# Optimization experiments

Hardware: AMD Instinct MI355X
Metric: run time of the kernel (lower is better)

## Reference

```python
import jax, jax.numpy as jnp
import numpy as np

NUM_HEADS = 4
HEAD_DIM = 64  # out_dim // num_heads = 256 // 4
NEG_SLOPE = 0.2


def setup_inputs() -> dict:
    key = jax.random.key(0)
    k1, k2 = jax.random.split(key)
    h = jax.random.normal(k1, (8, 2048, 256), dtype=jnp.float32)
    # Linear(in_dim, head_dim*num_heads, bias=False): store as [in_dim, out_dim]
    W = jax.random.normal(k2, (256, 256), dtype=jnp.float32) * (1.0 / np.sqrt(256.0))
    return {"h": h, "W": W}


def reference(h, W):
    B, T, _ = h.shape
    # Wh: (B, H, T, D)
    Wh = (h @ W).reshape(B, T, NUM_HEADS, HEAD_DIM).transpose(0, 2, 1, 3)
    scale = 1.0 / (HEAD_DIM ** 0.5)
    # full T x T scores per head, LeakyReLU then softmax over keys
    scores = jnp.einsum('bhtd,bhsd->bhts', Wh, Wh) * scale
    attention = jax.nn.softmax(jax.nn.leaky_relu(scores, negative_slope=NEG_SLOPE), axis=-1)
    h_prime = jnp.einsum('bhts,bhsd->bhtd', attention, Wh)
    # concat=True: (B, T, H*D)
    return h_prime.transpose(0, 2, 1, 3).reshape(B, T, NUM_HEADS * HEAD_DIM)
```

## Files before the change

kernel.cpp:

```cpp
#include <hip/hip_runtime.h>

#define T_SEQ 2048
#define NH 4
#define DH 64

typedef __bf16 bf16x8 __attribute__((ext_vector_type(8)));
typedef float f32x4 __attribute__((ext_vector_type(4)));
typedef unsigned short u16x8 __attribute__((ext_vector_type(8)));

__device__ __forceinline__ unsigned short f2bf_rne(float x) {
  unsigned int u = __builtin_bit_cast(unsigned int, x);
  u += 0x7fffu + ((u >> 16) & 1u);
  return (unsigned short)(u >> 16);
}
__device__ __forceinline__ float bf2f(unsigned short s) {
  unsigned int u = ((unsigned int)s) << 16;
  return __builtin_bit_cast(float, u);
}

__global__ void prep_w(const float* __restrict__ W,
                       unsigned short* __restrict__ WtHi,
                       unsigned short* __restrict__ WtLo) {
  __shared__ float ls[32][65];
  const int tid = threadIdx.x;
  const int k0 = (blockIdx.x >> 2) * 32;
  const int n0 = (blockIdx.x & 3) * 64;
#pragma unroll
  for (int i = 0; i < 8; i++) {
    int e = i * 256 + tid;
    int r = e >> 6, c = e & 63;
    ls[r][c] = W[(k0 + r) * 256 + n0 + c];
  }
  __syncthreads();
  const int n = tid & 63;
  const int part = tid >> 6;
  u16x8 vh, vl;
#pragma unroll
  for (int j = 0; j < 8; j++) {
    float w = ls[part * 8 + j][n];
    unsigned short h16 = f2bf_rne(w);
    vh[j] = h16;
    vl[j] = f2bf_rne(w - bf2f(h16));
  }
  size_t dst = (size_t)(n0 + n) * 256 + k0 + part * 8;
  *(u16x8*)&WtHi[dst] = vh;
  *(u16x8*)&WtLo[dst] = vl;
}

__global__ __launch_bounds__(256, 2) void wh_gemm(
    const float* __restrict__ h,
    const unsigned short* __restrict__ WtHi,
    const unsigned short* __restrict__ WtLo,
    unsigned short* __restrict__ Kb, unsigned short* __restrict__ Vs) {
  __shared__ __align__(16) unsigned short ktile[32][272];
  __shared__ __align__(16) unsigned short vtile[256][40];
  const int tid = threadIdx.x;
  const int wave = tid >> 6, lane = tid & 63, l15 = lane & 15, quad = lane >> 4;
  const int m0b = blockIdx.x * 32;
  const int m0 = m0b + (wave & 1) * 16;
  const int n0w = (wave >> 1) * 128;
  f32x4 acc[8];
#pragma unroll
  for (int nt = 0; nt < 8; nt++) acc[nt] = (f32x4){0.f, 0.f, 0.f, 0.f};

  for (int kc = 0; kc < 8; kc++) {
    const float4* hp = (const float4*)&h[(size_t)(m0 + l15) * 256 + kc * 32 + quad * 8];
    float4 a0 = hp[0], a1 = hp[1];
    float xs[8] = {a0.x, a0.y, a0.z, a0.w, a1.x, a1.y, a1.z, a1.w};
    u16x8 ah, al;
#pragma unroll
    for (int j = 0; j < 8; j++) {
      unsigned short h16 = f2bf_rne(xs[j]);
      ah[j] = h16;
      al[j] = f2bf_rne(xs[j] - bf2f(h16));
    }
    bf16x8 ahi = __builtin_bit_cast(bf16x8, ah);
    bf16x8 alo = __builtin_bit_cast(bf16x8, al);
#pragma unroll
    for (int nt = 0; nt < 8; nt++) {
      size_t wb = (size_t)(n0w + nt * 16 + l15) * 256 + kc * 32 + quad * 8;
      bf16x8 bhi = *(const bf16x8*)&WtHi[wb];
      bf16x8 blo = *(const bf16x8*)&WtLo[wb];
      acc[nt] = __builtin_amdgcn_mfma_f32_16x16x32_bf16(ahi, bhi, acc[nt], 0, 0, 0);
      acc[nt] = __builtin_amdgcn_mfma_f32_16x16x32_bf16(alo, bhi, acc[nt], 0, 0, 0);
      acc[nt] = __builtin_amdgcn_mfma_f32_16x16x32_bf16(ahi, blo, acc[nt], 0, 0, 0);
    }
  }
  const float s1 = 0.424664717f;
  const int tl = (wave & 1) * 16 + quad * 4;
#pragma unroll
  for (int nt = 0; nt < 8; nt++) {
    int n = n0w + nt * 16 + l15;
    ushort4 vp;
#pragma unroll
    for (int r = 0; r < 4; r++) {
      float v = acc[nt][r];
      ktile[tl + r][n] = f2bf_rne(v * s1);
      ((unsigned short*)&vp)[r] = f2bf_rne(v);
    }
    *(uint2*)&vtile[n][tl] = __builtin_bit_cast(uint2, vp);
  }
  __syncthreads();
  {
    int t = tid >> 3, seg = tid & 7;
    int m = m0b + t, b = m >> 11, tt = m & 2047;
    int head = seg >> 1, d0 = (seg & 1) * 32;
    unsigned short* dst = &Kb[((size_t)(b * NH + head) * T_SEQ + tt) * DH + d0];
#pragma unroll
    for (int q = 0; q < 4; q++)
      *(u16x8*)&dst[q * 8] = *(const u16x8*)&ktile[t][seg * 32 + q * 8];
  }
  {
    int n = tid, head = n >> 6, d = n & 63;
    int b = m0b >> 11, t0 = m0b & 2047;
    unsigned short* dst = &Vs[((size_t)(b * NH + head) * DH + d) * T_SEQ + t0];
#pragma unroll
    for (int q = 0; q < 4; q++) {
      uint2 lo = *(const uint2*)&vtile[n][q * 4];
      uint2 hi = *(const uint2*)&vtile[n][16 + q * 4];
      uint4 pk = {lo.x, lo.y, hi.x, hi.y};
      *(uint4*)&dst[q * 8] = pk;
    }
  }
}

__global__ __launch_bounds__(256, 3) void attn(
    const unsigned short* __restrict__ Kb, const unsigned short* __restrict__ Vs,
    float* __restrict__ out) {
  __shared__ __align__(16) float cbuf[2][64 * 68];
  __shared__ float lbuf[4][64];
  __shared__ float inv_s[64];
  const int tid = threadIdx.x, wave = tid >> 6, lane = tid & 63;
  const int l15 = lane & 15, quad = lane >> 4;
  const int bh = blockIdx.x & 31;
  const int qt = blockIdx.x >> 5;
  const int q0 = qt * 64;
  const unsigned short* Kbh = Kb + (size_t)bh * T_SEQ * DH;
  const unsigned short* Vbh = Vs + (size_t)bh * DH * T_SEQ;

  bf16x8 bq[4][2];
#pragma unroll
  for (int nt = 0; nt < 4; nt++)
#pragma unroll
    for (int kc = 0; kc < 2; kc++)
      bq[nt][kc] = *(const bf16x8*)&Kbh[(size_t)(q0 + nt * 16 + l15) * DH + kc * 32 + quad * 8];

  f32x4 o[4][4];
  float lsum[4] = {0.f, 0.f, 0.f, 0.f};
#pragma unroll
  for (int mt = 0; mt < 4; mt++)
#pragma unroll
    for (int dt = 0; dt < 4; dt++) o[mt][dt] = (f32x4){0.f, 0.f, 0.f, 0.f};

  const int sbase = wave * 512;
  bf16x8 ka[2][2], vb[4];
#pragma unroll
  for (int mt = 0; mt < 2; mt++)
#pragma unroll
    for (int kc = 0; kc < 2; kc++)
      ka[mt][kc] = *(const bf16x8*)&Kbh[(size_t)(sbase + mt * 16 + l15) * DH + kc * 32 + quad * 8];
#pragma unroll
  for (int dt = 0; dt < 4; dt++)
    vb[dt] = *(const bf16x8*)&Vbh[(size_t)(dt * 16 + l15) * T_SEQ + sbase + quad * 8];

  for (int it = 0; it < 16; it++) {
    const int nxt = sbase + ((it == 15) ? it : it + 1) * 32;
    f32x4 s[2][4];
#pragma unroll
    for (int mt = 0; mt < 2; mt++)
#pragma unroll
      for (int nt = 0; nt < 4; nt++) {
        f32x4 c = {0.f, 0.f, 0.f, 0.f};
        c = __builtin_amdgcn_mfma_f32_16x16x32_bf16(ka[mt][0], bq[nt][0], c, 0, 0, 0);
        c = __builtin_amdgcn_mfma_f32_16x16x32_bf16(ka[mt][1], bq[nt][1], c, 0, 0, 0);
        s[mt][nt] = c;
      }
#pragma unroll
    for (int mt = 0; mt < 2; mt++)
#pragma unroll
      for (int kc = 0; kc < 2; kc++)
        ka[mt][kc] = *(const bf16x8*)&Kbh[(size_t)(nxt + mt * 16 + l15) * DH + kc * 32 + quad * 8];

    uint2 pk[2][4];
#pragma unroll
    for (int mt = 0; mt < 2; mt++)
#pragma unroll
      for (int nt = 0; nt < 4; nt++) {
        float v0 = s[mt][nt][0], v1 = s[mt][nt][1];
        float v2 = s[mt][nt][2], v3 = s[mt][nt][3];
        float e0 = __builtin_amdgcn_exp2f(fmaxf(v0, 0.2f * v0));
        float e1 = __builtin_amdgcn_exp2f(fmaxf(v1, 0.2f * v1));
        float e2 = __builtin_amdgcn_exp2f(fmaxf(v2, 0.2f * v2));
        float e3 = __builtin_amdgcn_exp2f(fmaxf(v3, 0.2f * v3));
        lsum[nt] += (e0 + e1) + (e2 + e3);
        pk[mt][nt].x = (__builtin_bit_cast(unsigned int, e1) & 0xffff0000u) |
                       (__builtin_bit_cast(unsigned int, e0) >> 16);
        pk[mt][nt].y = (__builtin_bit_cast(unsigned int, e3) & 0xffff0000u) |
                       (__builtin_bit_cast(unsigned int, e2) >> 16);
      }

#pragma unroll
    for (int mq = 0; mq < 4; mq++) {
      uint4 pu = {pk[0][mq].x, pk[0][mq].y, pk[1][mq].x, pk[1][mq].y};
      bf16x8 pa = __builtin_bit_cast(bf16x8, pu);
#pragma unroll
      for (int dt = 0; dt < 4; dt++)
        o[mq][dt] = __builtin_amdgcn_mfma_f32_16x16x32_bf16(pa, vb[dt], o[mq][dt], 0, 0, 0);
    }
#pragma unroll
    for (int dt = 0; dt < 4; dt++)
      vb[dt] = *(const bf16x8*)&Vbh[(size_t)(dt * 16 + l15) * T_SEQ + nxt + quad * 8];
  }

#pragma unroll
  for (int nt = 0; nt < 4; nt++) {
    float l = lsum[nt];
    l += __shfl_xor(l, 16, 64);
    l += __shfl_xor(l, 32, 64);
    if (quad == 0) lbuf[wave][nt * 16 + l15] = l;
  }
  __syncthreads();
  if (wave >= 2) {
    float* cb = cbuf[wave - 2];
#pragma unroll
    for (int mt = 0; mt < 4; mt++)
#pragma unroll
      for (int dt = 0; dt < 4; dt++)
        *(f32x4*)&cb[(dt * 16 + l15) * 68 + mt * 16 + quad * 4] = o[mt][dt];
  }
  if (wave == 0) {
    float s = lbuf[0][lane] + lbuf[1][lane] + lbuf[2][lane] + lbuf[3][lane];
    inv_s[lane] = 1.0f / s;
  }
  __syncthreads();
  if (wave < 2) {
    float* cb = cbuf[wave];
#pragma unroll
    for (int mt = 0; mt < 4; mt++)
#pragma unroll
      for (int dt = 0; dt < 4; dt++)
        o[mt][dt] += *(const f32x4*)&cb[(dt * 16 + l15) * 68 + mt * 16 + quad * 4];
  }
  __syncthreads();
  if (wave == 1) {
#pragma unroll
    for (int mt = 0; mt < 4; mt++)
#pragma unroll
      for (int dt = 0; dt < 4; dt++)
        *(f32x4*)&cbuf[0][(dt * 16 + l15) * 68 + mt * 16 + quad * 4] = o[mt][dt];
  }
  __syncthreads();
  if (wave == 0) {
#pragma unroll
    for (int mt = 0; mt < 4; mt++)
#pragma unroll
      for (int dt = 0; dt < 4; dt++)
        o[mt][dt] += *(const f32x4*)&cbuf[0][(dt * 16 + l15) * 68 + mt * 16 + quad * 4];
    const int b = bh >> 2, head = bh & 3;
#pragma unroll
    for (int mt = 0; mt < 4; mt++) {
#pragma unroll
      for (int r = 0; r < 4; r++) {
        int q = mt * 16 + quad * 4 + r;
        float iv = inv_s[q];
        float* dst = &out[((size_t)b * T_SEQ + q0 + q) * 256 + head * 64];
#pragma unroll
        for (int dt = 0; dt < 4; dt++) dst[dt * 16 + l15] = o[mt][dt][r] * iv;
      }
    }
  }
}

extern "C" void kernel_launch(void* const* d_in, const int* in_sizes, int n_in,
                              void* d_out, int out_size, void* d_ws, size_t ws_size,
                              hipStream_t stream) {
  const float* h = (const float*)d_in[0];
  const float* W = (const float*)d_in[1];
  float* out = (float*)d_out;
  unsigned short* Kb = (unsigned short*)d_ws;
  unsigned short* Vs = Kb + (size_t)32 * T_SEQ * DH;
  unsigned short* WtHi = (unsigned short*)out;
  unsigned short* WtLo = WtHi + 65536;
  prep_w<<<32, 256, 0, stream>>>(W, WtHi, WtLo);
  wh_gemm<<<512, 256, 0, stream>>>(h, WtHi, WtLo, Kb, Vs);
  attn<<<1024, 256, 0, stream>>>(Kb, Vs, out);
}
```

Measured before the change: 182.0 us.

## Switch attention to fp16 MFMA with fixed exp shift and MFMA row sums

K and V are now stored as fp16 instead of bf16, and the attention kernel uses f16 MFMA. A constant shift of -14 is seeded into the score accumulator (scaled by 0.2 on the negative branch) so the exponentials stay within fp16 range, and they are packed with cvt_pkrtz instead of manual bit truncation. The per-lane scalar row-sum adds and shuffle reduction are replaced by an extra MFMA against a ones vector, whose result goes through the same cross-wave LDS reduction as the output. This trims VALU work in the softmax inner loop and adds one MFMA per query tile, but it relies on the fixed shift keeping fp16 from overflowing or underflowing for these input ranges.

```diff
diff --git a/kernel.cpp b/kernel.cpp
--- a/kernel.cpp
+++ b/kernel.cpp
@@ -5,6 +5,8 @@
 #define DH 64
 
 typedef __bf16 bf16x8 __attribute__((ext_vector_type(8)));
+typedef _Float16 f16x8 __attribute__((ext_vector_type(8)));
+typedef _Float16 f16x2 __attribute__((ext_vector_type(2)));
 typedef float f32x4 __attribute__((ext_vector_type(4)));
 typedef unsigned short u16x8 __attribute__((ext_vector_type(8)));
 
@@ -16,6 +18,10 @@
 __device__ __forceinline__ float bf2f(unsigned short s) {
   unsigned int u = ((unsigned int)s) << 16;
   return __builtin_bit_cast(float, u);
+}
+__device__ __forceinline__ unsigned short f2h(float x) {
+  _Float16 h = (_Float16)x;
+  return __builtin_bit_cast(unsigned short, h);
 }
 
 __global__ void prep_w(const float* __restrict__ W,
@@ -95,8 +101,8 @@
 #pragma unroll
     for (int r = 0; r < 4; r++) {
       float v = acc[nt][r];
-      ktile[tl + r][n] = f2bf_rne(v * s1);
-      ((unsigned short*)&vp)[r] = f2bf_rne(v);
+      ktile[tl + r][n] = f2h(v * s1);
+      ((unsigned short*)&vp)[r] = f2h(v);
     }
     *(uint2*)&vtile[n][tl] = __builtin_bit_cast(uint2, vp);
   }
@@ -127,9 +133,7 @@
 __global__ __launch_bounds__(256, 3) void attn(
     const unsigned short* __restrict__ Kb, const unsigned short* __restrict__ Vs,
     float* __restrict__ out) {
-  __shared__ __align__(16) float cbuf[2][64 * 68];
-  __shared__ float lbuf[4][64];
-  __shared__ float inv_s[64];
+  __shared__ __align__(16) float cbuf[2][80 * 68];
   const int tid = threadIdx.x, wave = tid >> 6, lane = tid & 63;
   const int l15 = lane & 15, quad = lane >> 4;
   const int bh = blockIdx.x & 31;
@@ -138,30 +142,36 @@
   const unsigned short* Kbh = Kb + (size_t)bh * T_SEQ * DH;
   const unsigned short* Vbh = Vs + (size_t)bh * DH * T_SEQ;
 
-  bf16x8 bq[4][2];
+  f16x8 bq[4][2];
 #pragma unroll
   for (int nt = 0; nt < 4; nt++)
 #pragma unroll
     for (int kc = 0; kc < 2; kc++)
-      bq[nt][kc] = *(const bf16x8*)&Kbh[(size_t)(q0 + nt * 16 + l15) * DH + kc * 32 + quad * 8];
-
-  f32x4 o[4][4];
-  float lsum[4] = {0.f, 0.f, 0.f, 0.f};
-#pragma unroll
-  for (int mt = 0; mt < 4; mt++)
+      bq[nt][kc] = *(const f16x8*)&Kbh[(size_t)(q0 + nt * 16 + l15) * DH + kc * 32 + quad * 8];
+
+  f16x8 ones;
+#pragma unroll
+  for (int j = 0; j < 8; j++) ones[j] = (_Float16)1.0f;
+
+  f32x4 o[4][4], lacc[4];
+#pragma unroll
+  for (int mt = 0; mt < 4; mt++) {
+    lacc[mt] = (f32x4){0.f, 0.f, 0.f, 0.f};
 #pragma unroll
     for (int dt = 0; dt < 4; dt++) o[mt][dt] = (f32x4){0.f, 0.f, 0.f, 0.f};
+  }
+  const f32x4 cinit = {-14.f, -14.f, -14.f, -14.f};
 
   const int sbase = wave * 512;
-  bf16x8 ka[2][2], vb[4];
+  f16x8 ka[2][2], vb[4];
 #pragma unroll
   for (int mt = 0; mt < 2; mt++)
 #pragma unroll
     for (int kc = 0; kc < 2; kc++)
-      ka[mt][kc] = *(const bf16x8*)&Kbh[(size_t)(sbase + mt * 16 + l15) * DH + kc * 32 + quad * 8];
+      ka[mt][kc] = *(const f16x8*)&Kbh[(size_t)(sbase + mt * 16 + l15) * DH + kc * 32 + quad * 8];
 #pragma unroll
   for (int dt = 0; dt < 4; dt++)
-    vb[dt] = *(const bf16x8*)&Vbh[(size_t)(dt * 16 + l15) * T_SEQ + sbase + quad * 8];
+    vb[dt] = *(const f16x8*)&Vbh[(size_t)(dt * 16 + l15) * T_SEQ + sbase + quad * 8];
 
   for (int it = 0; it < 16; it++) {
     const int nxt = sbase + ((it == 15) ? it : it + 1) * 32;
@@ -170,99 +180,93 @@
     for (int mt = 0; mt < 2; mt++)
 #pragma unroll
       for (int nt = 0; nt < 4; nt++) {
-        f32x4 c = {0.f, 0.f, 0.f, 0.f};
-        c = __builtin_amdgcn_mfma_f32_16x16x32_bf16(ka[mt][0], bq[nt][0], c, 0, 0, 0);
-        c = __builtin_amdgcn_mfma_f32_16x16x32_bf16(ka[mt][1], bq[nt][1], c, 0, 0, 0);
+        f32x4 c = __builtin_amdgcn_mfma_f32_16x16x32_f16(ka[mt][0], bq[nt][0], cinit, 0, 0, 0);
+        c = __builtin_amdgcn_mfma_f32_16x16x32_f16(ka[mt][1], bq[nt][1], c, 0, 0, 0);
         s[mt][nt] = c;
       }
 #pragma unroll
     for (int mt = 0; mt < 2; mt++)
 #pragma unroll
       for (int kc = 0; kc < 2; kc++)
-        ka[mt][kc] = *(const bf16x8*)&Kbh[(size_t)(nxt + mt * 16 + l15) * DH + kc * 32 + quad * 8];
-
-    uint2 pk[2][4];
+        ka[mt][kc] = *(const f16x8*)&Kbh[(size_t)(nxt + mt * 16 + l15) * DH + kc * 32 + quad * 8];
+
+    unsigned int pk[2][4][2];
 #pragma unroll
     for (int mt = 0; mt < 2; mt++)
 #pragma unroll
       for (int nt = 0; nt < 4; nt++) {
-        float v0 = s[mt][nt][0], v1 = s[mt][nt][1];
-        float v2 = s[mt][nt][2], v3 = s[mt][nt][3];
-        float e0 = __builtin_amdgcn_exp2f(fmaxf(v0, 0.2f * v0));
-        float e1 = __builtin_amdgcn_exp2f(fmaxf(v1, 0.2f * v1));
-        float e2 = __builtin_amdgcn_exp2f(fmaxf(v2, 0.2f * v2));
-        float e3 = __builtin_amdgcn_exp2f(fmaxf(v3, 0.2f * v3));
-        lsum[nt] += (e0 + e1) + (e2 + e3);
-        pk[mt][nt].x = (__builtin_bit_cast(unsigned int, e1) & 0xffff0000u) |
-                       (__builtin_bit_cast(unsigned int, e0) >> 16);
-        pk[mt][nt].y = (__builtin_bit_cast(unsigned int, e3) & 0xffff0000u) |
-                       (__builtin_bit_cast(unsigned int, e2) >> 16);
+        float e[4];
+#pragma unroll
+        for (int r = 0; r < 4; r++) {
+          float u = s[mt][nt][r];
+          e[r] = __builtin_amdgcn_exp2f(fmaxf(u, __builtin_fmaf(0.2f, u, -11.2f)));
+        }
+        pk[mt][nt][0] = __builtin_bit_cast(unsigned int, __builtin_amdgcn_cvt_pkrtz(e[0], e[1]));
+        pk[mt][nt][1] = __builtin_bit_cast(unsigned int, __builtin_amdgcn_cvt_pkrtz(e[2], e[3]));
       }
 
 #pragma unroll
     for (int mq = 0; mq < 4; mq++) {
-      uint4 pu = {pk[0][mq].x, pk[0][mq].y, pk[1][mq].x, pk[1][mq].y};
-      bf16x8 pa = __builtin_bit_cast(bf16x8, pu);
-#pragma unroll
-      for (int dt = 0; dt < 4; dt++)
-        o[mq][dt] = __builtin_amdgcn_mfma_f32_16x16x32_bf16(pa, vb[dt], o[mq][dt], 0, 0, 0);
+      uint4 pu = {pk[0][mq][0], pk[0][mq][1], pk[1][mq][0], pk[1][mq][1]};
+      f16x8 pa = __builtin_bit_cast(f16x8, pu);
+#pragma unroll
+      for (int dt = 0; dt < 4; dt++)
+        o[mq][dt] = __builtin_amdgcn_mfma_f32_16x16x32_f16(pa, vb[dt], o[mq][dt], 0, 0, 0);
+      lacc[mq] = __builtin_amdgcn_mfma_f32_16x16x32_f16(pa, ones, lacc[mq], 0, 0, 0);
     }
 #pragma unroll
     for (int dt = 0; dt < 4; dt++)
-      vb[dt] = *(const bf16x8*)&Vbh[(size_t)(dt * 16 + l15) * T_SEQ + nxt + quad * 8];
-  }
-
-#pragma unroll
-  for (int nt = 0; nt < 4; nt++) {
-    float l = lsum[nt];
-    l += __shfl_xor(l, 16, 64);
-    l += __shfl_xor(l, 32, 64);
-    if (quad == 0) lbuf[wave][nt * 16 + l15] = l;
-  }
+      vb[dt] = *(const f16x8*)&Vbh[(size_t)(dt * 16 + l15) * T_SEQ + nxt + quad * 8];
+  }
+
   __syncthreads();
   if (wave >= 2) {
     float* cb = cbuf[wave - 2];
 #pragma unroll
-    for (int mt = 0; mt < 4; mt++)
+    for (int mt = 0; mt < 4; mt++) {
 #pragma unroll
       for (int dt = 0; dt < 4; dt++)
         *(f32x4*)&cb[(dt * 16 + l15) * 68 + mt * 16 + quad * 4] = o[mt][dt];
-  }
-  if (wave == 0) {
-    float s = lbuf[0][lane] + lbuf[1][lane] + lbuf[2][lane] + lbuf[3][lane];
-    inv_s[lane] = 1.0f / s;
+      *(f32x4*)&cb[(64 + l15) * 68 + mt * 16 + quad * 4] = lacc[mt];
+    }
   }
   __syncthreads();
   if (wave < 2) {
     float* cb = cbuf[wave];
 #pragma unroll
-    for (int mt = 0; mt < 4; mt++)
+    for (int mt = 0; mt < 4; mt++) {
 #pragma unroll
       for (int dt = 0; dt < 4; dt++)
         o[mt][dt] += *(const f32x4*)&cb[(dt * 16 + l15) * 68 + mt * 16 + quad * 4];
+      lacc[mt] += *(const f32x4*)&cb[(64 + l15) * 68 + mt * 16 + quad * 4];
+    }
   }
   __syncthreads();
   if (wave == 1) {
 #pragma unroll
-    for (int mt = 0; mt < 4; mt++)
+    for (int mt = 0; mt < 4; mt++) {
 #pragma unroll
       for (int dt = 0; dt < 4; dt++)
         *(f32x4*)&cbuf[0][(dt * 16 + l15) * 68 + mt * 16 + quad * 4] = o[mt][dt];
+      *(f32x4*)&cbuf[0][(64 + l15) * 68 + mt * 16 + quad * 4] = lacc[mt];
+    }
   }
   __syncthreads();
   if (wave == 0) {
 #pragma unroll
-    for (int mt = 0; mt < 4; mt++)
+    for (int mt = 0; mt < 4; mt++) {
 #pragma unroll
       for (int dt = 0; dt < 4; dt++)
         o[mt][dt] += *(const f32x4*)&cbuf[0][(dt * 16 + l15) * 68 + mt * 16 + quad * 4];
+      lacc[mt] += *(const f32x4*)&cbuf[0][(64 + l15) * 68 + mt * 16 + quad * 4];
+    }
     const int b = bh >> 2, head = bh & 3;
 #pragma unroll
     for (int mt = 0; mt < 4; mt++) {
 #pragma unroll
       for (int r = 0; r < 4; r++) {
+        float iv = 1.0f / lacc[mt][r];
         int q = mt * 16 + quad * 4 + r;
-        float iv = inv_s[q];
         float* dst = &out[((size_t)b * T_SEQ + q0 + q) * 256 + head * 64];
 #pragma unroll
         for (int dt = 0; dt < 4; dt++) dst[dt * 16 + l15] = o[mt][dt][r] * iv;
```

Result: slower. 252.9 us (+38.9%).

## Switch attention operands to fp16 with shifted scores and interleaved per-tile softmax

Applied to the files above, without the earlier changes.

K and V are stored as fp16 instead of bf16, and the attention MFMAs use the f16 variant. Scores start from a constant negative accumulator with a matching offset in the LeakyReLU branch, which shifts exponents into fp16 range. The probabilities are then packed with cvt_pkrtz. The loop is restructured so each query tile's QK, exp and PV are interleaved, to overlap MFMA with VALU work and reduce live registers. Trade-offs: fp16 range assumptions on the scores, and round-toward-zero packing of probabilities.

```diff
diff --git a/kernel.cpp b/kernel.cpp
--- a/kernel.cpp
+++ b/kernel.cpp
@@ -5,6 +5,7 @@
 #define DH 64
 
 typedef __bf16 bf16x8 __attribute__((ext_vector_type(8)));
+typedef _Float16 f16x8 __attribute__((ext_vector_type(8)));
 typedef float f32x4 __attribute__((ext_vector_type(4)));
 typedef unsigned short u16x8 __attribute__((ext_vector_type(8)));
 
@@ -16,6 +17,10 @@
 __device__ __forceinline__ float bf2f(unsigned short s) {
   unsigned int u = ((unsigned int)s) << 16;
   return __builtin_bit_cast(float, u);
+}
+__device__ __forceinline__ unsigned short f2h(float x) {
+  _Float16 h = (_Float16)x;
+  return __builtin_bit_cast(unsigned short, h);
 }
 
 __global__ void prep_w(const float* __restrict__ W,
@@ -95,8 +100,8 @@
 #pragma unroll
     for (int r = 0; r < 4; r++) {
       float v = acc[nt][r];
-      ktile[tl + r][n] = f2bf_rne(v * s1);
-      ((unsigned short*)&vp)[r] = f2bf_rne(v);
+      ktile[tl + r][n] = f2h(v * s1);
+      ((unsigned short*)&vp)[r] = f2h(v);
     }
     *(uint2*)&vtile[n][tl] = __builtin_bit_cast(uint2, vp);
   }
@@ -138,12 +143,12 @@
   const unsigned short* Kbh = Kb + (size_t)bh * T_SEQ * DH;
   const unsigned short* Vbh = Vs + (size_t)bh * DH * T_SEQ;
 
-  bf16x8 bq[4][2];
+  f16x8 bq[4][2];
 #pragma unroll
   for (int nt = 0; nt < 4; nt++)
 #pragma unroll
     for (int kc = 0; kc < 2; kc++)
-      bq[nt][kc] = *(const bf16x8*)&Kbh[(size_t)(q0 + nt * 16 + l15) * DH + kc * 32 + quad * 8];
+      bq[nt][kc] = *(const f16x8*)&Kbh[(size_t)(q0 + nt * 16 + l15) * DH + kc * 32 + quad * 8];
 
   f32x4 o[4][4];
   float lsum[4] = {0.f, 0.f, 0.f, 0.f};
@@ -151,65 +156,64 @@
   for (int mt = 0; mt < 4; mt++)
 #pragma unroll
     for (int dt = 0; dt < 4; dt++) o[mt][dt] = (f32x4){0.f, 0.f, 0.f, 0.f};
+  const f32x4 cinit = {-14.f, -14.f, -14.f, -14.f};
 
   const int sbase = wave * 512;
-  bf16x8 ka[2][2], vb[4];
+  f16x8 ka[2][2], vb[4];
 #pragma unroll
   for (int mt = 0; mt < 2; mt++)
 #pragma unroll
     for (int kc = 0; kc < 2; kc++)
-      ka[mt][kc] = *(const bf16x8*)&Kbh[(size_t)(sbase + mt * 16 + l15) * DH + kc * 32 + quad * 8];
+      ka[mt][kc] = *(const f16x8*)&Kbh[(size_t)(sbase + mt * 16 + l15) * DH + kc * 32 + quad * 8];
 #pragma unroll
   for (int dt = 0; dt < 4; dt++)
-    vb[dt] = *(const bf16x8*)&Vbh[(size_t)(dt * 16 + l15) * T_SEQ + sbase + quad * 8];
+    vb[dt] = *(const f16x8*)&Vbh[(size_t)(dt * 16 + l15) * T_SEQ + sbase + quad * 8];
 
   for (int it = 0; it < 16; it++) {
     const int nxt = sbase + ((it == 15) ? it : it + 1) * 32;
-    f32x4 s[2][4];
-#pragma unroll
-    for (int mt = 0; mt < 2; mt++)
-#pragma unroll
-      for (int nt = 0; nt < 4; nt++) {
-        f32x4 c = {0.f, 0.f, 0.f, 0.f};
-        c = __builtin_amdgcn_mfma_f32_16x16x32_bf16(ka[mt][0], bq[nt][0], c, 0, 0, 0);
-        c = __builtin_amdgcn_mfma_f32_16x16x32_bf16(ka[mt][1], bq[nt][1], c, 0, 0, 0);
-        s[mt][nt] = c;
-      }
-#pragma unroll
-    for (int mt = 0; mt < 2; mt++)
-#pragma unroll
-      for (int kc = 0; kc < 2; kc++)
-        ka[mt][kc] = *(const bf16x8*)&Kbh[(size_t)(nxt + mt * 16 + l15) * DH + kc * 32 + quad * 8];
-
-    uint2 pk[2][4];
-#pragma unroll
-    for (int mt = 0; mt < 2; mt++)
-#pragma unroll
-      for (int nt = 0; nt < 4; nt++) {
-        float v0 = s[mt][nt][0], v1 = s[mt][nt][1];
-        float v2 = s[mt][nt][2], v3 = s[mt][nt][3];
-        float e0 = __builtin_amdgcn_exp2f(fmaxf(v0, 0.2f * v0));
-        float e1 = __builtin_amdgcn_exp2f(fmaxf(v1, 0.2f * v1));
-        float e2 = __builtin_amdgcn_exp2f(fmaxf(v2, 0.2f * v2));
-        float e3 = __builtin_amdgcn_exp2f(fmaxf(v3, 0.2f * v3));
-        lsum[nt] += (e0 + e1) + (e2 + e3);
-        pk[mt][nt].x = (__builtin_bit_cast(unsigned int, e1) & 0xffff0000u) |
-                       (__builtin_bit_cast(unsigned int, e0) >> 16);
-        pk[mt][nt].y = (__builtin_bit_cast(unsigned int, e3) & 0xffff0000u) |
-                       (__builtin_bit_cast(unsigned int, e2) >> 16);
-      }
-
-#pragma unroll
-    for (int mq = 0; mq < 4; mq++) {
-      uint4 pu = {pk[0][mq].x, pk[0][mq].y, pk[1][mq].x, pk[1][mq].y};
-      bf16x8 pa = __builtin_bit_cast(bf16x8, pu);
-#pragma unroll
-      for (int dt = 0; dt < 4; dt++)
-        o[mq][dt] = __builtin_amdgcn_mfma_f32_16x16x32_bf16(pa, vb[dt], o[mq][dt], 0, 0, 0);
-    }
-#pragma unroll
-    for (int dt = 0; dt < 4; dt++)
-      vb[dt] = *(const bf16x8*)&Vbh[(size_t)(dt * 16 + l15) * T_SEQ + nxt + quad * 8];
+#pragma unroll
+    for (int nt = 0; nt < 4; nt++) {
+      f32x4 s0 = __builtin_amdgcn_mfma_f32_16x16x32_f16(ka[0][0], bq[nt][0], cinit, 0, 0, 0);
+      s0 = __builtin_amdgcn_mfma_f32_16x16x32_f16(ka[0][1], bq[nt][1], s0, 0, 0, 0);
+      f32x4 s1 = __builtin_amdgcn_mfma_f32_16x16x32_f16(ka[1][0], bq[nt][0], cinit, 0, 0, 0);
+      s1 = __builtin_amdgcn_mfma_f32_16x16x32_f16(ka[1][1], bq[nt][1], s1, 0, 0, 0);
+
+      float e0, e1, e2, e3, f0, f1, f2, f3;
+      {
+        float u;
+        u = s0[0]; e0 = __builtin_amdgcn_exp2f(fmaxf(u, __builtin_fmaf(0.2f, u, -11.2f)));
+        u = s0[1]; e1 = __builtin_amdgcn_exp2f(fmaxf(u, __builtin_fmaf(0.2f, u, -11.2f)));
+        u = s0[2]; e2 = __builtin_amdgcn_exp2f(fmaxf(u, __builtin_fmaf(0.2f, u, -11.2f)));
+        u = s0[3]; e3 = __builtin_amdgcn_exp2f(fmaxf(u, __builtin_fmaf(0.2f, u, -11.2f)));
+        u = s1[0]; f0 = __builtin_amdgcn_exp2f(fmaxf(u, __builtin_fmaf(0.2f, u, -11.2f)));
+        u = s1[1]; f1 = __builtin_amdgcn_exp2f(fmaxf(u, __builtin_fmaf(0.2f, u, -11.2f)));
+        u = s1[2]; f2 = __builtin_amdgcn_exp2f(fmaxf(u, __builtin_fmaf(0.2f, u, -11.2f)));
+        u = s1[3]; f3 = __builtin_amdgcn_exp2f(fmaxf(u, __builtin_fmaf(0.2f, u, -11.2f)));
+      }
+      lsum[nt] += ((e0 + e1) + (e2 + e3)) + ((f0 + f1) + (f2 + f3));
+      uint4 pu;
+      pu.x = __builtin_bit_cast(unsigned int, __builtin_amdgcn_cvt_pkrtz(e0, e1));
+      pu.y = __builtin_bit_cast(unsigned int, __builtin_amdgcn_cvt_pkrtz(e2, e3));
+      pu.z = __builtin_bit_cast(unsigned int, __builtin_amdgcn_cvt_pkrtz(f0, f1));
+      pu.w = __builtin_bit_cast(unsigned int, __builtin_amdgcn_cvt_pkrtz(f2, f3));
+      f16x8 pa = __builtin_bit_cast(f16x8, pu);
+
+      if (nt == 3) {
+#pragma unroll
+        for (int mt = 0; mt < 2; mt++)
+#pragma unroll
+          for (int kc = 0; kc < 2; kc++)
+            ka[mt][kc] = *(const f16x8*)&Kbh[(size_t)(nxt + mt * 16 + l15) * DH + kc * 32 + quad * 8];
+      }
+#pragma unroll
+      for (int dt = 0; dt < 4; dt++)
+        o[nt][dt] = __builtin_amdgcn_mfma_f32_16x16x32_f16(pa, vb[dt], o[nt][dt], 0, 0, 0);
+      if (nt == 3) {
+#pragma unroll
+        for (int dt = 0; dt < 4; dt++)
+          vb[dt] = *(const f16x8*)&Vbh[(size_t)(dt * 16 + l15) * T_SEQ + nxt + quad * 8];
+      }
+    }
   }
 
 #pragma unroll
@@ -261,8 +265,8 @@
     for (int mt = 0; mt < 4; mt++) {
 #pragma unroll
       for (int r = 0; r < 4; r++) {
+        float iv = inv_s[mt * 16 + quad * 4 + r];
         int q = mt * 16 + quad * 4 + r;
-        float iv = inv_s[q];
         float* dst = &out[((size_t)b * T_SEQ + q0 + q) * 256 + head * 64];
 #pragma unroll
         for (int dt = 0; dt < 4; dt++) dst[dt * 16 + l15] = o[mt][dt][r] * iv;
```

New measurement: 173.6 us. -4.6%, faster.
